# Performance work log

Measured on AMD Instinct MI355X. Metric: run time of the kernel, lower is better.

## Reference

```python
import jax, jax.numpy as jnp
import numpy as np

M_IND = 1024   # inducing points
K_NN = 16      # nearest neighbors
JITTER = 1e-4


def rbf(X, Z):
    # unit-variance, unit-lengthscale RBF kernel; returns (K, squared distances)
    sq = jnp.sum(X * X, -1)[:, None] + jnp.sum(Z * Z, -1)[None, :] - 2.0 * (X @ Z.T)
    sq = jnp.maximum(sq, 0.0)
    return jnp.exp(-0.5 * sq), sq


def setup_inputs() -> dict:
    key = jax.random.key(0)
    k1, k2, k3 = jax.random.split(key, 3)
    return {
        "X": jax.random.normal(k1, (65536, 3), jnp.float32),
        "Z": jax.random.normal(k2, (M_IND, 3), jnp.float32),
        "Lu_raw": jax.random.normal(k3, (M_IND, M_IND), jnp.float32),
        "mu": jnp.zeros((M_IND,), jnp.float32),
    }


def reference(X, Z, Lu_raw, mu):
    N = X.shape[0]
    Kxx = jnp.ones((N,), X.dtype)                      # diag of RBF(X,X) is 1
    Kxz, dist = rbf(X, Z)                              # [N,M], [N,M]
    Kzz, _ = rbf(Z, Z)                                 # [M,M]

    # transform_to(lower_cholesky): strict lower triangle + exp(diag)
    Lu = jnp.tril(Lu_raw, -1) + jnp.diag(jnp.exp(jnp.diag(Lu_raw)))

    eyeM = jnp.eye(M_IND, dtype=X.dtype)
    L = jnp.linalg.cholesky(Kzz + JITTER * eyeM)       # [M,M]
    Kzz_j = L @ L.T                                    # == little_L @ little_L.T math (Kzz + jitter*I)
    Su = Lu @ Lu.T                                     # full variational covariance

    # K nearest inducing points per data point (argsort(dist)[:, :K])
    _, idx = jax.lax.top_k(-dist, K_NN)                # [N,K]

    lKzz = Kzz_j[idx[:, :, None], idx[:, None, :]]     # [N,K,K] gathered submatrices
    lS = Su[idx[:, :, None], idx[:, None, :]]          # [N,K,K]
    lKxz = jnp.take_along_axis(Kxz, idx, axis=1)       # [N,K]
    lmu = mu[idx]                                      # [N,K]

    eyeK = jnp.eye(K_NN, dtype=X.dtype)
    inv = jnp.linalg.inv(lKzz + JITTER * eyeK)         # batched tiny inverses [N,K,K]
    W = jnp.einsum('nk,nkj->nj', lKxz, inv)            # [N,K]

    mean = jnp.einsum('nk,nk->n', W, lmu)              # [N]
    cov = (Kxx
           - jnp.einsum('ni,nij,nj->n', W, lKzz, W)
           + jnp.einsum('ni,nij,nj->n', W, lS, W))
    std = jnp.sqrt(jnp.clip(cov, 0.05, None))          # qF scale = clamp(cov, 0.05)**0.5
    return jnp.stack([mean, std])                      # [2,N] qF parameters
```

## Files before the change

### kernel.cpp

```cpp
#include <hip/hip_runtime.h>
#include <math.h>

#define N_PTS 65536
#define M_IND 1024
#define KNN 16
#define JITTER 1e-4f

#define PACKED_FLOATS (M_IND * (M_IND + 1) / 2)
#define PACKED_BYTES  ((size_t)PACKED_FLOATS * sizeof(float))

#define TSU 32
#define SU_BLOCKS 528
#define PTS_PER_BLK 128
#define QSTRIDE 17
#define GRID_BLKS (N_PTS / PTS_PER_BLK)


__device__ __forceinline__ void su_tile(const float* __restrict__ Lu_raw,
                                        float* __restrict__ P,
                                        int bid, int tid,
                                        float (*As)[36], float (*Bs)[36]) {
    int rt = (int)((sqrtf(8.0f * (float)bid + 1.0f) - 1.0f) * 0.5f);
    while ((rt + 1) * (rt + 2) / 2 <= bid) ++rt;
    while (rt * (rt + 1) / 2 > bid) --rt;
    int ct = bid - rt * (rt + 1) / 2;
    int i0 = rt * TSU, j0 = ct * TSU;

    int tx = tid & 15, ty = tid >> 4;
    int sr = tid >> 3, sc = (tid & 7) << 2;
    float a00 = 0.f, a01 = 0.f, a10 = 0.f, a11 = 0.f;

    int nch = ct + 1;
    int gi = i0 + sr, gj = j0 + sr;
    float4 pa = *(const float4*)(Lu_raw + (unsigned)gi * M_IND + sc);
    float4 pb = *(const float4*)(Lu_raw + (unsigned)gj * M_IND + sc);

    for (int c = 0; c < nch; ++c) {
        int gk = (c << 5) + sc;
        float aa[4] = {pa.x, pa.y, pa.z, pa.w};
        float bb[4] = {pb.x, pb.y, pb.z, pb.w};
        #pragma unroll
        for (int q = 0; q < 4; ++q) {
            int k = gk + q;
            aa[q] = (k < gi) ? aa[q] : ((k == gi) ? __expf(aa[q]) : 0.0f);
            bb[q] = (k < gj) ? bb[q] : ((k == gj) ? __expf(bb[q]) : 0.0f);
        }
        *(float4*)&As[sr][sc] = make_float4(aa[0], aa[1], aa[2], aa[3]);
        *(float4*)&Bs[sr][sc] = make_float4(bb[0], bb[1], bb[2], bb[3]);
        __syncthreads();
        if (c + 1 < nch) {
            int kn = ((c + 1) << 5) + sc;
            pa = *(const float4*)(Lu_raw + (unsigned)gi * M_IND + kn);
            pb = *(const float4*)(Lu_raw + (unsigned)gj * M_IND + kn);
        }
        #pragma unroll
        for (int kk = 0; kk < 32; kk += 4) {
            float4 av0 = *(const float4*)&As[ty][kk];
            float4 av1 = *(const float4*)&As[ty + 16][kk];
            float4 bv0 = *(const float4*)&Bs[tx][kk];
            float4 bv1 = *(const float4*)&Bs[tx + 16][kk];
            a00 = fmaf(av0.x, bv0.x, fmaf(av0.y, bv0.y, fmaf(av0.z, bv0.z, fmaf(av0.w, bv0.w, a00))));
            a01 = fmaf(av0.x, bv1.x, fmaf(av0.y, bv1.y, fmaf(av0.z, bv1.z, fmaf(av0.w, bv1.w, a01))));
            a10 = fmaf(av1.x, bv0.x, fmaf(av1.y, bv0.y, fmaf(av1.z, bv0.z, fmaf(av1.w, bv0.w, a10))));
            a11 = fmaf(av1.x, bv1.x, fmaf(av1.y, bv1.y, fmaf(av1.z, bv1.z, fmaf(av1.w, bv1.w, a11))));
        }
        __syncthreads();
    }

    int ia = i0 + ty, ib = i0 + ty + 16;
    int ja = j0 + tx, jb = j0 + tx + 16;
    if (ja <= ia) P[((unsigned)ia * (ia + 1) >> 1) + ja] = a00;
    if (jb <= ia) P[((unsigned)ia * (ia + 1) >> 1) + jb] = a01;
    if (ja <= ib) P[((unsigned)ib * (ib + 1) >> 1) + ja] = a10;
    if (jb <= ib) P[((unsigned)ib * (ib + 1) >> 1) + jb] = a11;
}

__global__ __launch_bounds__(256) void su_kernel(const float* __restrict__ Lu_raw,
                                                 float* __restrict__ P) {
    __shared__ float As[TSU][36];
    __shared__ float Bs[TSU][36];
    su_tile(Lu_raw, P, blockIdx.x, threadIdx.x, As, Bs);
}

__device__ __forceinline__ void ce(unsigned long long& x, unsigned long long& y) {
    unsigned long long a = x, b = y;
    bool c = a < b;
    x = c ? a : b;
    y = c ? b : a;
}
__device__ __forceinline__ void ce(float& x, float& y) {
    float a = fminf(x, y), b = fmaxf(x, y);
    x = a; y = b;
}

template <typename KT>
__device__ __forceinline__ void sort16(KT* a) {
    #pragma unroll
    for (int p = 1; p < 16; p <<= 1)
        #pragma unroll
        for (int k = p; k >= 1; k >>= 1)
            #pragma unroll
            for (int j = k & (p - 1); j + k < 16; j += 2 * k)
                #pragma unroll
                for (int i = 0; i < k; ++i)
                    if (i + j + k < 16)
                        if (((i + j) / (2 * p)) == ((i + j + k) / (2 * p)))
                            ce(a[i + j], a[i + j + k]);
}

template <typename KT>
__device__ __forceinline__ void cleanup16(KT* a) {
    #pragma unroll
    for (int d = 8; d >= 1; d >>= 1)
        #pragma unroll
        for (int i = 0; i < 16; ++i)
            if ((i & d) == 0) ce(a[i], a[i | d]);
}

__device__ __forceinline__ float uval(float4 z, float xn0, float xn1, float xn2) {
    return fmaf(xn0, z.x, fmaf(xn1, z.y, fmaf(xn2, z.z, z.w)));
}

template <int MODE>
__global__ __launch_bounds__(256, 2) void vnngp_kernel(const float* __restrict__ X,
                                                       const float* __restrict__ Z,
                                                       const float* __restrict__ mu,
                                                       float* __restrict__ P,
                                                       const float* __restrict__ Lu_raw,
                                                       unsigned int* __restrict__ ctr,
                                                       float* __restrict__ out) {
    __shared__ __align__(16) char smem[37888];
    float4* Zs = (float4*)smem;
    float* mus = (float*)(smem + 16384);
    unsigned long long* qb = (unsigned long long*)(smem + 20480);
    int tid = threadIdx.x;

    for (int r = tid; r < M_IND; r += 256) {
        float zx = Z[r * 3 + 0], zy = Z[r * 3 + 1], zz = Z[r * 3 + 2];
        Zs[r] = make_float4(zx, zy, zz, 0.5f * (zx * zx + zy * zy + zz * zz));
        mus[r] = mu[r];
    }

    if (MODE == 2) {
        float (*As)[36] = (float (*)[36])(smem + 20480);
        float (*Bs)[36] = (float (*)[36])(smem + 20480 + 4608);
        int t = blockIdx.x;
        #pragma unroll
        for (int r = 16; r < 32; ++r) {
            int s = (r * (r + 1)) >> 1;
            if (t >= s) ++t;
        }
        su_tile(Lu_raw, P, t, tid, As, Bs);
        if (blockIdx.x < 16) {
            int r = 16 + blockIdx.x;
            su_tile(Lu_raw, P, (r * (r + 1)) >> 1, tid, As, Bs);
        }
        __syncthreads();
        if (tid == 0) {
            __threadfence();
            atomicAdd(ctr, 1u);
        }
    } else {
        __syncthreads();
    }

    {
        int pt = tid >> 2, sub = tid & 3;
        int nA = blockIdx.x * PTS_PER_BLK + pt;
        int nB = nA + 64;
        float xA0 = X[nA * 3 + 0], xA1 = X[nA * 3 + 1], xA2 = X[nA * 3 + 2];
        float xB0 = X[nB * 3 + 0], xB1 = X[nB * 3 + 1], xB2 = X[nB * 3 + 2];
        float xqA = fmaf(xA0, xA0, fmaf(xA1, xA1, xA2 * xA2));
        float xqB = fmaf(xB0, xB0, fmaf(xB1, xB1, xB2 * xB2));
        float nA0 = -xA0, nA1 = -xA1, nA2 = -xA2;
        float nB0 = -xB0, nB1 = -xB1, nB2 = -xB2;
        int mbase = sub << 8;
        int rot = sub << 1;

        float TA[16], TB[16];
        #pragma unroll
        for (int j = 0; j < 16; ++j) { TA[j] = 3.4e38f; TB[j] = 3.4e38f; }
        #pragma unroll 1
        for (int c = 0; c < 16; ++c) {
            int base = mbase + (c << 4);
            #pragma unroll
            for (int j = 0; j < 16; ++j) {
                int m = base + ((j + rot) & 15);
                float4 z = Zs[m];
                TA[j] = fminf(TA[j], uval(z, nA0, nA1, nA2));
                TB[j] = fminf(TB[j], uval(z, nB0, nB1, nB2));
            }
        }
        sort16(TA);
        sort16(TB);
        #pragma unroll
        for (int round = 1; round <= 2; round <<= 1) {
            float oA[16], oB[16];
            #pragma unroll
            for (int i = 0; i < 16; ++i) {
                oA[i] = __shfl_xor(TA[i], round, 64);
                oB[i] = __shfl_xor(TB[i], round, 64);
            }
            #pragma unroll
            for (int i = 0; i < 16; ++i) {
                TA[i] = fminf(TA[i], oA[15 - i]);
                TB[i] = fminf(TB[i], oB[15 - i]);
            }
            cleanup16(TA);
            cleanup16(TB);
        }
        float TstarA = TA[15], TstarB = TB[15];

        unsigned short* mycA = ((unsigned short*)qb) + pt * (QSTRIDE * 4) + sub * 16;
        unsigned short* mycB = ((unsigned short*)qb) + (pt + 64) * (QSTRIDE * 4) + sub * 16;
        int cntA = 0, cntB = 0;
        #pragma unroll 1
        for (int c = 0; c < 16; ++c) {
            int base = mbase + (c << 4);
            #pragma unroll
            for (int j = 0; j < 16; ++j) {
                int m = base + ((j + rot) & 15);
                float4 z = Zs[m];
                float uA = uval(z, nA0, nA1, nA2);
                float uB = uval(z, nB0, nB1, nB2);
                if (uA <= TstarA) { if (cntA < 16) mycA[cntA] = (unsigned short)m; ++cntA; }
                if (uB <= TstarB) { if (cntB < 16) mycB[cntB] = (unsigned short)m; ++cntB; }
            }
        }

        int ovfA = cntA > 16 ? 1 : 0;
        ovfA |= __shfl_xor(ovfA, 1, 64);
        ovfA |= __shfl_xor(ovfA, 2, 64);
        int ovfB = cntB > 16 ? 1 : 0;
        ovfB |= __shfl_xor(ovfB, 1, 64);
        ovfB |= __shfl_xor(ovfB, 2, 64);

        if (!ovfA) {
            const unsigned long long* m64 = (const unsigned long long*)mycA;
            unsigned long long raw[4] = {m64[0], m64[1], m64[2], m64[3]};
            unsigned long long C[16];
            #pragma unroll
            for (int i = 0; i < 16; ++i) {
                int m = (int)((raw[i >> 2] >> ((i & 3) * 16)) & 0x3FF);
                float u = uval(Zs[m], nA0, nA1, nA2);
                float d = fmaxf(fmaf(2.0f, u, xqA), 0.0f);
                unsigned long long key =
                    ((unsigned long long)__float_as_uint(d) << 32) | (unsigned)m;
                C[i] = (i < cntA) ? key : ~0ULL;
            }
            sort16(C);
            #pragma unroll
            for (int round = 1; round <= 2; round <<= 1) {
                unsigned long long o[16];
                #pragma unroll
                for (int i = 0; i < 16; ++i) o[i] = __shfl_xor(C[i], round, 64);
                #pragma unroll
                for (int i = 0; i < 16; ++i) {
                    unsigned long long b = o[15 - i];
                    C[i] = C[i] < b ? C[i] : b;
                }
                cleanup16(C);
            }
            if (sub == 0) {
                #pragma unroll
                for (int i = 0; i < 16; ++i) qb[pt * QSTRIDE + i] = C[i];
            }
        } else if (sub == 0) {
            unsigned long long R[16];
            #pragma unroll
            for (int i = 0; i < 16; ++i) R[i] = ~0ULL;
            for (int m = 0; m < M_IND; ++m) {
                float u = uval(Zs[m], nA0, nA1, nA2);
                float d = fmaxf(fmaf(2.0f, u, xqA), 0.0f);
                unsigned long long kk =
                    ((unsigned long long)__float_as_uint(d) << 32) | (unsigned)m;
                if (kk < R[15]) {
                    #pragma unroll
                    for (int j = 0; j < 16; ++j) {
                        unsigned long long t = R[j];
                        bool cc = kk < t;
                        R[j] = cc ? kk : t;
                        kk = cc ? t : kk;
                    }
                }
            }
            #pragma unroll
            for (int i = 0; i < 16; ++i) qb[pt * QSTRIDE + i] = R[i];
        }

        if (!ovfB) {
            const unsigned long long* m64 = (const unsigned long long*)mycB;
            unsigned long long raw[4] = {m64[0], m64[1], m64[2], m64[3]};
            unsigned long long C[16];
            #pragma unroll
            for (int i = 0; i < 16; ++i) {
                int m = (int)((raw[i >> 2] >> ((i & 3) * 16)) & 0x3FF);
                float u = uval(Zs[m], nB0, nB1, nB2);
                float d = fmaxf(fmaf(2.0f, u, xqB), 0.0f);
                unsigned long long key =
                    ((unsigned long long)__float_as_uint(d) << 32) | (unsigned)m;
                C[i] = (i < cntB) ? key : ~0ULL;
            }
            sort16(C);
            #pragma unroll
            for (int round = 1; round <= 2; round <<= 1) {
                unsigned long long o[16];
                #pragma unroll
                for (int i = 0; i < 16; ++i) o[i] = __shfl_xor(C[i], round, 64);
                #pragma unroll
                for (int i = 0; i < 16; ++i) {
                    unsigned long long b = o[15 - i];
                    C[i] = C[i] < b ? C[i] : b;
                }
                cleanup16(C);
            }
            if (sub == 0) {
                #pragma unroll
                for (int i = 0; i < 16; ++i) qb[(pt + 64) * QSTRIDE + i] = C[i];
            }
        } else if (sub == 0) {
            unsigned long long R[16];
            #pragma unroll
            for (int i = 0; i < 16; ++i) R[i] = ~0ULL;
            for (int m = 0; m < M_IND; ++m) {
                float u = uval(Zs[m], nB0, nB1, nB2);
                float d = fmaxf(fmaf(2.0f, u, xqB), 0.0f);
                unsigned long long kk =
                    ((unsigned long long)__float_as_uint(d) << 32) | (unsigned)m;
                if (kk < R[15]) {
                    #pragma unroll
                    for (int j = 0; j < 16; ++j) {
                        unsigned long long t = R[j];
                        bool cc = kk < t;
                        R[j] = cc ? kk : t;
                        kk = cc ? t : kk;
                    }
                }
            }
            #pragma unroll
            for (int i = 0; i < 16; ++i) qb[(pt + 64) * QSTRIDE + i] = R[i];
        }
    }
    __syncthreads();

    if (MODE == 2) {
        if (tid == 0) {
            while (__hip_atomic_load(ctr, __ATOMIC_ACQUIRE, __HIP_MEMORY_SCOPE_AGENT)
                   < (unsigned)GRID_BLKS)
                __builtin_amdgcn_s_sleep(8);
        }
        __syncthreads();
    }

    int role = tid >> 7;
    int pt2 = tid & 127;
    int n = blockIdx.x * PTS_PER_BLK + pt2;
    int idx[KNN];
    float kv[KNN];
    float nx[KNN], ny[KNN], nz[KNN], nq[KNN];
    #pragma unroll
    for (int a = 0; a < KNN; ++a) {
        unsigned long long k = qb[pt2 * QSTRIDE + a];
        idx[a] = (int)(k & 0xFFFFFFFFULL);
        float d = __uint_as_float((unsigned)(k >> 32));
        kv[a] = __expf(-0.5f * d);
        float4 z = Zs[idx[a]];
        nx[a] = z.x; ny[a] = z.y; nz[a] = z.z; nq[a] = z.w;
    }
    __syncthreads();

    float A[KNN * (KNN + 1) / 2];
    #pragma unroll
    for (int r = 0; r < KNN; ++r) {
        A[r * (r + 1) / 2 + r] = 1.0f + 2.0f * JITTER;
        #pragma unroll
        for (int c = 0; c < r; ++c) {
            float dot = fmaf(nx[r], nx[c], fmaf(ny[r], ny[c], nz[r] * nz[c]));
            A[r * (r + 1) / 2 + c] = __expf(fminf(dot - nq[r] - nq[c], 0.0f));
        }
    }

    #pragma unroll
    for (int c = 0; c < KNN; ++c) {
        float diag = A[c * (c + 1) / 2 + c];
        #pragma unroll
        for (int k = 0; k < c; ++k) {
            float l = A[c * (c + 1) / 2 + k];
            diag = fmaf(-l, l, diag);
        }
        float rinv = __frsqrt_rn(fmaxf(diag, 1e-12f));
        A[c * (c + 1) / 2 + c] = rinv;
        #pragma unroll
        for (int r = c + 1; r < KNN; ++r) {
            float v = A[r * (r + 1) / 2 + c];
            #pragma unroll
            for (int k = 0; k < c; ++k)
                v = fmaf(-A[r * (r + 1) / 2 + k], A[c * (c + 1) / 2 + k], v);
            A[r * (r + 1) / 2 + c] = v * rinv;
        }
    }

    float w[KNN];
    #pragma unroll
    for (int r = 0; r < KNN; ++r) {
        float v = kv[r];
        #pragma unroll
        for (int c = 0; c < r; ++c) v = fmaf(-A[r * (r + 1) / 2 + c], w[c], v);
        w[r] = v * A[r * (r + 1) / 2 + r];
    }
    #pragma unroll
    for (int r = KNN - 1; r >= 0; --r) {
        float v = w[r];
        #pragma unroll
        for (int c = r + 1; c < KNN; ++c) v = fmaf(-A[c * (c + 1) / 2 + r], w[c], v);
        w[r] = v * A[r * (r + 1) / 2 + r];
    }

    float wk = 0.f, ww = 0.f, mean = 0.f;
    #pragma unroll
    for (int a = 0; a < KNN; ++a) {
        wk = fmaf(w[a], kv[a], wk);
        ww = fmaf(w[a], w[a], ww);
        mean = fmaf(w[a], mus[idx[a]], mean);
    }

    float qs_p = 0.f;
    if (MODE != 0) {
        #pragma unroll
        for (int r = 0; r < KNN; ++r) {
            if ((r & 1) == role) {
                int a = idx[r];
                float wr = w[r];
                float rowacc = 0.f;
                #pragma unroll
                for (int c = 0; c < r; ++c) {
                    int b = idx[c];
                    int hi = a > b ? a : b;
                    int lo = a > b ? b : a;
                    rowacc = fmaf(w[c], P[((unsigned)hi * (hi + 1) >> 1) + lo], rowacc);
                }
                qs_p = fmaf(wr, fmaf(wr, P[((unsigned)a * (a + 1) >> 1) + a], 2.0f * rowacc), qs_p);
            }
        }
    } else if (role == 0) {
        int si[KNN]; float sw[KNN];
        #pragma unroll
        for (int a = 0; a < KNN; ++a) { si[a] = idx[a]; sw[a] = w[a]; }
        #pragma unroll
        for (int a = 1; a < KNN; ++a) {
            int iv = si[a]; float wv = sw[a];
            int b = a - 1;
            while (b >= 0 && si[b] > iv) { si[b + 1] = si[b]; sw[b + 1] = sw[b]; --b; }
            si[b + 1] = iv; sw[b + 1] = wv;
        }
        int s = 0;
        int kend = si[KNN - 1];
        for (int k = 0; k <= kend; ++k) {
            float v = 0.f;
            if (s < KNN && si[s] == k) {
                v = sw[s] * __expf(Lu_raw[(unsigned)k * M_IND + k]);
                ++s;
            }
            for (int a = s; a < KNN; ++a)
                v = fmaf(sw[a], Lu_raw[(unsigned)si[a] * M_IND + k], v);
            qs_p = fmaf(v, v, qs_p);
        }
    }

    float* xch = (float*)qb;
    if (role == 1) xch[pt2] = qs_p;
    __syncthreads();
    if (role == 0) {
        float qs = qs_p + xch[pt2];
        float cov = 1.0f - (wk - JITTER * ww) + qs;
        float sd = sqrtf(fmaxf(cov, 0.05f));
        out[n] = mean;
        out[N_PTS + n] = sd;
    }
}

extern "C" void kernel_launch(void* const* d_in, const int* in_sizes, int n_in,
                              void* d_out, int out_size, void* d_ws, size_t ws_size,
                              hipStream_t stream) {
    const float* X      = (const float*)d_in[0];
    const float* Z      = (const float*)d_in[1];
    const float* Lu_raw = (const float*)d_in[2];
    const float* mu     = (const float*)d_in[3];
    float* out = (float*)d_out;

    if (ws_size >= PACKED_BYTES + 64) {
        float* P = (float*)d_ws;
        unsigned int* ctr = (unsigned int*)((char*)d_ws + PACKED_BYTES);
        hipMemsetAsync(ctr, 0, sizeof(unsigned int), stream);
        vnngp_kernel<2><<<GRID_BLKS, 256, 0, stream>>>(X, Z, mu, P, Lu_raw, ctr, out);
    } else if (ws_size >= PACKED_BYTES) {
        float* P = (float*)d_ws;
        su_kernel<<<SU_BLOCKS, 256, 0, stream>>>(Lu_raw, P);
        vnngp_kernel<1><<<GRID_BLKS, 256, 0, stream>>>(X, Z, mu, P, Lu_raw, nullptr, out);
    } else {
        vnngp_kernel<0><<<GRID_BLKS, 256, 0, stream>>>(X, Z, mu, nullptr, Lu_raw, nullptr, out);
    }
}
```

Measured before the change: 163.6 us.

## Split Su build and cooperative 4-lane per-point Cholesky into separate kernels

Replaces the fused persistent kernel, which built packed Su inside the grid and spin-waited on a global counter, with a separate su_kernel launch followed by a new selection-plus-solve kernel. The new kernel uses 8 lanes per point for top-k selection over 128 inducing points each, with a threshold filter pass and a full-scan fallback on overflow. It then splits each point's 16x16 Cholesky, triangular solves and the Su quadratic form across 4 lanes using shuffles, with 4 blocks per CU instead of 2. This removes the grid-wide spin barrier and cuts per-thread register load. In exchange it adds a second launch and extra shuffle traffic.

```diff
diff --git a/kernel.cpp b/kernel.cpp
--- a/kernel.cpp
+++ b/kernel.cpp
@@ -119,6 +119,394 @@
 
 __device__ __forceinline__ float uval(float4 z, float xn0, float xn1, float xn2) {
     return fmaf(xn0, z.x, fmaf(xn1, z.y, fmaf(xn2, z.z, z.w)));
+}
+
+#define LI0(c) ((c) & 3)
+#define LI1(c) ((c) & 7)
+#define LI2(c) ((c) < 12 ? (c) : 0)
+
+__global__ __launch_bounds__(256, 4) void selp2_kernel(const float* __restrict__ X,
+                                                       const float* __restrict__ Z,
+                                                       const float* __restrict__ mu,
+                                                       const float* __restrict__ P,
+                                                       float* __restrict__ out) {
+    __shared__ __align__(16) char smem[36864];
+    float4* Zs = (float4*)smem;
+    float* mus = (float*)(smem + 16384);
+    unsigned long long* qb = (unsigned long long*)(smem + 20480);
+    int tid = threadIdx.x;
+
+    for (int r = tid; r < M_IND; r += 256) {
+        float zx = Z[r * 3 + 0], zy = Z[r * 3 + 1], zz = Z[r * 3 + 2];
+        Zs[r] = make_float4(zx, zy, zz, 0.5f * (zx * zx + zy * zy + zz * zz));
+        mus[r] = mu[r];
+    }
+    __syncthreads();
+
+    {
+        int oct = tid >> 3, sub = tid & 7;
+        int nA = blockIdx.x * 64 + oct;
+        int nB = nA + 32;
+        float xA0 = X[nA * 3 + 0], xA1 = X[nA * 3 + 1], xA2 = X[nA * 3 + 2];
+        float xB0 = X[nB * 3 + 0], xB1 = X[nB * 3 + 1], xB2 = X[nB * 3 + 2];
+        float xqA = fmaf(xA0, xA0, fmaf(xA1, xA1, xA2 * xA2));
+        float xqB = fmaf(xB0, xB0, fmaf(xB1, xB1, xB2 * xB2));
+        float mA0 = -xA0, mA1 = -xA1, mA2 = -xA2;
+        float mB0 = -xB0, mB1 = -xB1, mB2 = -xB2;
+        int mbase = sub << 7;
+        int rot = sub << 1;
+
+        float TA[16], TB[16];
+        #pragma unroll
+        for (int j = 0; j < 16; ++j) { TA[j] = 3.4e38f; TB[j] = 3.4e38f; }
+        #pragma unroll 1
+        for (int c = 0; c < 8; ++c) {
+            int base = mbase + (c << 4);
+            #pragma unroll
+            for (int j = 0; j < 16; ++j) {
+                int m = base + ((j + rot) & 15);
+                float4 z = Zs[m];
+                TA[j] = fminf(TA[j], uval(z, mA0, mA1, mA2));
+                TB[j] = fminf(TB[j], uval(z, mB0, mB1, mB2));
+            }
+        }
+        sort16(TA);
+        sort16(TB);
+        #pragma unroll
+        for (int round = 1; round <= 4; round <<= 1) {
+            float oA[16], oB[16];
+            #pragma unroll
+            for (int i = 0; i < 16; ++i) {
+                oA[i] = __shfl_xor(TA[i], round, 64);
+                oB[i] = __shfl_xor(TB[i], round, 64);
+            }
+            #pragma unroll
+            for (int i = 0; i < 16; ++i) {
+                TA[i] = fminf(TA[i], oA[15 - i]);
+                TB[i] = fminf(TB[i], oB[15 - i]);
+            }
+            cleanup16(TA);
+            cleanup16(TB);
+        }
+        float TstarA = TA[15], TstarB = TB[15];
+
+        unsigned short* mycA = ((unsigned short*)qb) + oct * 128 + sub * 16;
+        unsigned short* mycB = ((unsigned short*)qb) + (oct + 32) * 128 + sub * 16;
+        int cntA = 0, cntB = 0;
+        #pragma unroll 1
+        for (int c = 0; c < 8; ++c) {
+            int base = mbase + (c << 4);
+            #pragma unroll
+            for (int j = 0; j < 16; ++j) {
+                int m = base + ((j + rot) & 15);
+                float4 z = Zs[m];
+                float uA = uval(z, mA0, mA1, mA2);
+                float uB = uval(z, mB0, mB1, mB2);
+                if (uA <= TstarA) { if (cntA < 16) mycA[cntA] = (unsigned short)m; ++cntA; }
+                if (uB <= TstarB) { if (cntB < 16) mycB[cntB] = (unsigned short)m; ++cntB; }
+            }
+        }
+
+        int ovfA = cntA > 16 ? 1 : 0;
+        ovfA |= __shfl_xor(ovfA, 1, 64);
+        ovfA |= __shfl_xor(ovfA, 2, 64);
+        ovfA |= __shfl_xor(ovfA, 4, 64);
+        int ovfB = cntB > 16 ? 1 : 0;
+        ovfB |= __shfl_xor(ovfB, 1, 64);
+        ovfB |= __shfl_xor(ovfB, 2, 64);
+        ovfB |= __shfl_xor(ovfB, 4, 64);
+
+        if (!ovfA) {
+            const unsigned long long* m64 = (const unsigned long long*)mycA;
+            unsigned long long raw[4] = {m64[0], m64[1], m64[2], m64[3]};
+            unsigned long long C[16];
+            #pragma unroll
+            for (int i = 0; i < 16; ++i) {
+                int m = (int)((raw[i >> 2] >> ((i & 3) * 16)) & 0x3FF);
+                float u = uval(Zs[m], mA0, mA1, mA2);
+                float d = fmaxf(fmaf(2.0f, u, xqA), 0.0f);
+                unsigned long long key =
+                    ((unsigned long long)__float_as_uint(d) << 32) | (unsigned)m;
+                C[i] = (i < cntA) ? key : ~0ULL;
+            }
+            sort16(C);
+            #pragma unroll
+            for (int round = 1; round <= 4; round <<= 1) {
+                unsigned long long o[16];
+                #pragma unroll
+                for (int i = 0; i < 16; ++i) o[i] = __shfl_xor(C[i], round, 64);
+                #pragma unroll
+                for (int i = 0; i < 16; ++i) {
+                    unsigned long long b = o[15 - i];
+                    C[i] = C[i] < b ? C[i] : b;
+                }
+                cleanup16(C);
+            }
+            if (sub == 0) {
+                #pragma unroll
+                for (int i = 0; i < 16; ++i) qb[oct * 32 + i] = C[i];
+            }
+        } else if (sub == 0) {
+            unsigned long long R[16];
+            #pragma unroll
+            for (int i = 0; i < 16; ++i) R[i] = ~0ULL;
+            for (int m = 0; m < M_IND; ++m) {
+                float u = uval(Zs[m], mA0, mA1, mA2);
+                float d = fmaxf(fmaf(2.0f, u, xqA), 0.0f);
+                unsigned long long kk =
+                    ((unsigned long long)__float_as_uint(d) << 32) | (unsigned)m;
+                if (kk < R[15]) {
+                    #pragma unroll
+                    for (int j = 0; j < 16; ++j) {
+                        unsigned long long t = R[j];
+                        bool cc = kk < t;
+                        R[j] = cc ? kk : t;
+                        kk = cc ? t : kk;
+                    }
+                }
+            }
+            #pragma unroll
+            for (int i = 0; i < 16; ++i) qb[oct * 32 + i] = R[i];
+        }
+
+        if (!ovfB) {
+            const unsigned long long* m64 = (const unsigned long long*)mycB;
+            unsigned long long raw[4] = {m64[0], m64[1], m64[2], m64[3]};
+            unsigned long long C[16];
+            #pragma unroll
+            for (int i = 0; i < 16; ++i) {
+                int m = (int)((raw[i >> 2] >> ((i & 3) * 16)) & 0x3FF);
+                float u = uval(Zs[m], mB0, mB1, mB2);
+                float d = fmaxf(fmaf(2.0f, u, xqB), 0.0f);
+                unsigned long long key =
+                    ((unsigned long long)__float_as_uint(d) << 32) | (unsigned)m;
+                C[i] = (i < cntB) ? key : ~0ULL;
+            }
+            sort16(C);
+            #pragma unroll
+            for (int round = 1; round <= 4; round <<= 1) {
+                unsigned long long o[16];
+                #pragma unroll
+                for (int i = 0; i < 16; ++i) o[i] = __shfl_xor(C[i], round, 64);
+                #pragma unroll
+                for (int i = 0; i < 16; ++i) {
+                    unsigned long long b = o[15 - i];
+                    C[i] = C[i] < b ? C[i] : b;
+                }
+                cleanup16(C);
+            }
+            if (sub == 0) {
+                #pragma unroll
+                for (int i = 0; i < 16; ++i) qb[(oct + 32) * 32 + i] = C[i];
+            }
+        } else if (sub == 0) {
+            unsigned long long R[16];
+            #pragma unroll
+            for (int i = 0; i < 16; ++i) R[i] = ~0ULL;
+            for (int m = 0; m < M_IND; ++m) {
+                float u = uval(Zs[m], mB0, mB1, mB2);
+                float d = fmaxf(fmaf(2.0f, u, xqB), 0.0f);
+                unsigned long long kk =
+                    ((unsigned long long)__float_as_uint(d) << 32) | (unsigned)m;
+                if (kk < R[15]) {
+                    #pragma unroll
+                    for (int j = 0; j < 16; ++j) {
+                        unsigned long long t = R[j];
+                        bool cc = kk < t;
+                        R[j] = cc ? kk : t;
+                        kk = cc ? t : kk;
+                    }
+                }
+            }
+            #pragma unroll
+            for (int i = 0; i < 16; ++i) qb[(oct + 32) * 32 + i] = R[i];
+        }
+    }
+    __syncthreads();
+
+    {
+        int g = tid >> 2, l = tid & 3;
+        int n = blockIdx.x * 64 + g;
+        int lanebase = (tid & 63) & ~3;
+
+        int idx[16];
+        int iown[4];
+        float kvown[4];
+        float4 zrown[4];
+        #pragma unroll
+        for (int a = 0; a < 16; ++a) {
+            unsigned long long k = qb[g * 32 + a];
+            int ia = (int)(k & 0xFFFFFFFFULL);
+            float d = __uint_as_float((unsigned)(k >> 32));
+            float kva = __expf(-0.5f * d);
+            idx[a] = ia;
+            if ((a & 3) == l) {
+                iown[a >> 2] = ia;
+                kvown[a >> 2] = kva;
+                zrown[a >> 2] = Zs[ia];
+            }
+        }
+
+        float L0[4], L1[8], L2[12], L3[16];
+        float dg[4];
+        #pragma unroll
+        for (int k = 0; k < 4; ++k) dg[k] = 1.0f + 2.0f * JITTER;
+        #pragma unroll
+        for (int c = 0; c < 16; ++c) {
+            float4 zc = Zs[idx[c]];
+            #pragma unroll
+            for (int k = 0; k < 4; ++k) {
+                if (c < 4 * (k + 1)) {
+                    int r = l + 4 * k;
+                    float dot = fmaf(zrown[k].x, zc.x,
+                                fmaf(zrown[k].y, zc.y, zrown[k].z * zc.z));
+                    float val = __expf(fminf(dot - zrown[k].w - zc.w, 0.0f));
+                    if (c < r) {
+                        if (k == 0) L0[LI0(c)] = val;
+                        else if (k == 1) L1[LI1(c)] = val;
+                        else if (k == 2) L2[LI2(c)] = val;
+                        else L3[c] = val;
+                    }
+                }
+            }
+        }
+
+        float rinvown[4];
+        #pragma unroll
+        for (int c = 0; c < 16; ++c) {
+            const int owner = c & 3, kc = c >> 2;
+            float dval = __shfl(dg[kc], lanebase + owner, 64);
+            float rinv = __frsqrt_rn(fmaxf(dval, 1e-12f));
+            if (l == owner) rinvown[kc] = rinv;
+            float cv[4];
+            #pragma unroll
+            for (int k = 0; k < 4; ++k) {
+                cv[k] = 0.f;
+                if (c < 4 * (k + 1)) {
+                    int r = l + 4 * k;
+                    if (r > c) {
+                        float v;
+                        if (k == 0) { v = L0[LI0(c)] * rinv; L0[LI0(c)] = v; }
+                        else if (k == 1) { v = L1[LI1(c)] * rinv; L1[LI1(c)] = v; }
+                        else if (k == 2) { v = L2[LI2(c)] * rinv; L2[LI2(c)] = v; }
+                        else { v = L3[c] * rinv; L3[c] = v; }
+                        cv[k] = v;
+                    }
+                }
+            }
+            #pragma unroll
+            for (int j = c + 1; j < 16; ++j) {
+                float colj = __shfl(cv[j >> 2], lanebase + (j & 3), 64);
+                #pragma unroll
+                for (int k = 0; k < 4; ++k) {
+                    if (j < 4 * (k + 1)) {
+                        int r = l + 4 * k;
+                        if (r > j) {
+                            float u = cv[k] * colj;
+                            if (k == 0) L0[LI0(j)] -= u;
+                            else if (k == 1) L1[LI1(j)] -= u;
+                            else if (k == 2) L2[LI2(j)] -= u;
+                            else L3[j] -= u;
+                        } else if (r == j) {
+                            dg[k] = fmaf(-colj, colj, dg[k]);
+                        }
+                    }
+                }
+            }
+        }
+
+        float acc[4];
+        #pragma unroll
+        for (int k = 0; k < 4; ++k) acc[k] = kvown[k];
+        float yown[4];
+        #pragma unroll
+        for (int r = 0; r < 16; ++r) {
+            const int owner = r & 3, kr = r >> 2;
+            float yr = __shfl(acc[kr] * rinvown[kr], lanebase + owner, 64);
+            if (l == owner) yown[kr] = yr;
+            #pragma unroll
+            for (int k = 0; k < 4; ++k) {
+                if (r < 4 * (k + 1)) {
+                    int rr = l + 4 * k;
+                    if (rr > r) {
+                        float lv;
+                        if (k == 0) lv = L0[LI0(r)];
+                        else if (k == 1) lv = L1[LI1(r)];
+                        else if (k == 2) lv = L2[LI2(r)];
+                        else lv = L3[r];
+                        acc[k] = fmaf(-lv, yr, acc[k]);
+                    }
+                }
+            }
+        }
+
+        float wfull[16];
+        float wown[4] = {0.f, 0.f, 0.f, 0.f};
+        #pragma unroll
+        for (int r = 15; r >= 0; --r) {
+            const int owner = r & 3, kr = r >> 2;
+            float contrib = 0.f;
+            #pragma unroll
+            for (int k = 0; k < 4; ++k) {
+                if (r < 4 * (k + 1)) {
+                    int j = l + 4 * k;
+                    if (j > r) {
+                        float lv;
+                        if (k == 0) lv = L0[LI0(r)];
+                        else if (k == 1) lv = L1[LI1(r)];
+                        else if (k == 2) lv = L2[LI2(r)];
+                        else lv = L3[r];
+                        contrib = fmaf(lv, wown[k], contrib);
+                    }
+                }
+            }
+            contrib += __shfl_xor(contrib, 1, 64);
+            contrib += __shfl_xor(contrib, 2, 64);
+            float wr = __shfl((yown[kr] - contrib) * rinvown[kr],
+                              lanebase + owner, 64);
+            wfull[r] = wr;
+            if (l == owner) wown[kr] = wr;
+        }
+
+        float wkp = 0.f, wwp = 0.f, mnp = 0.f;
+        #pragma unroll
+        for (int k = 0; k < 4; ++k) {
+            wkp = fmaf(wown[k], kvown[k], wkp);
+            wwp = fmaf(wown[k], wown[k], wwp);
+            mnp = fmaf(wown[k], mus[iown[k]], mnp);
+        }
+
+        float qsp = 0.f;
+        #pragma unroll
+        for (int k = 0; k < 4; ++k) {
+            int r = l + 4 * k;
+            int a = iown[k];
+            float wr = wown[k];
+            float rowacc = 0.f;
+            #pragma unroll
+            for (int c = 0; c < 15; ++c) {
+                if (c < r) {
+                    int b = idx[c];
+                    int hi = a > b ? a : b;
+                    int lo = a > b ? b : a;
+                    rowacc = fmaf(wfull[c], P[((unsigned)hi * (hi + 1) >> 1) + lo], rowacc);
+                }
+            }
+            qsp = fmaf(wr, fmaf(wr, P[((unsigned)a * (a + 1) >> 1) + a], 2.0f * rowacc), qsp);
+        }
+
+        wkp += __shfl_xor(wkp, 1, 64); wkp += __shfl_xor(wkp, 2, 64);
+        wwp += __shfl_xor(wwp, 1, 64); wwp += __shfl_xor(wwp, 2, 64);
+        mnp += __shfl_xor(mnp, 1, 64); mnp += __shfl_xor(mnp, 2, 64);
+        qsp += __shfl_xor(qsp, 1, 64); qsp += __shfl_xor(qsp, 2, 64);
+
+        if (l == 0) {
+            float cov = 1.0f - (wkp - JITTER * wwp) + qsp;
+            float sd = sqrtf(fmaxf(cov, 0.05f));
+            out[n] = mnp;
+            out[N_PTS + n] = sd;
+        }
+    }
 }
 
 template <int MODE>
@@ -140,29 +528,7 @@
         Zs[r] = make_float4(zx, zy, zz, 0.5f * (zx * zx + zy * zy + zz * zz));
         mus[r] = mu[r];
     }
-
-    if (MODE == 2) {
-        float (*As)[36] = (float (*)[36])(smem + 20480);
-        float (*Bs)[36] = (float (*)[36])(smem + 20480 + 4608);
-        int t = blockIdx.x;
-        #pragma unroll
-        for (int r = 16; r < 32; ++r) {
-            int s = (r * (r + 1)) >> 1;
-            if (t >= s) ++t;
-        }
-        su_tile(Lu_raw, P, t, tid, As, Bs);
-        if (blockIdx.x < 16) {
-            int r = 16 + blockIdx.x;
-            su_tile(Lu_raw, P, (r * (r + 1)) >> 1, tid, As, Bs);
-        }
-        __syncthreads();
-        if (tid == 0) {
-            __threadfence();
-            atomicAdd(ctr, 1u);
-        }
-    } else {
-        __syncthreads();
-    }
+    __syncthreads();
 
     {
         int pt = tid >> 2, sub = tid & 3;
@@ -343,15 +709,6 @@
     }
     __syncthreads();
 
-    if (MODE == 2) {
-        if (tid == 0) {
-            while (__hip_atomic_load(ctr, __ATOMIC_ACQUIRE, __HIP_MEMORY_SCOPE_AGENT)
-                   < (unsigned)GRID_BLKS)
-                __builtin_amdgcn_s_sleep(8);
-        }
-        __syncthreads();
-    }
-
     int role = tid >> 7;
     int pt2 = tid & 127;
     int n = blockIdx.x * PTS_PER_BLK + pt2;
@@ -385,8 +742,8 @@
         float diag = A[c * (c + 1) / 2 + c];
         #pragma unroll
         for (int k = 0; k < c; ++k) {
-            float l = A[c * (c + 1) / 2 + k];
-            diag = fmaf(-l, l, diag);
+            float lv = A[c * (c + 1) / 2 + k];
+            diag = fmaf(-lv, lv, diag);
         }
         float rinv = __frsqrt_rn(fmaxf(diag, 1e-12f));
         A[c * (c + 1) / 2 + c] = rinv;
@@ -425,24 +782,7 @@
     }
 
     float qs_p = 0.f;
-    if (MODE != 0) {
-        #pragma unroll
-        for (int r = 0; r < KNN; ++r) {
-            if ((r & 1) == role) {
-                int a = idx[r];
-                float wr = w[r];
-                float rowacc = 0.f;
-                #pragma unroll
-                for (int c = 0; c < r; ++c) {
-                    int b = idx[c];
-                    int hi = a > b ? a : b;
-                    int lo = a > b ? b : a;
-                    rowacc = fmaf(w[c], P[((unsigned)hi * (hi + 1) >> 1) + lo], rowacc);
-                }
-                qs_p = fmaf(wr, fmaf(wr, P[((unsigned)a * (a + 1) >> 1) + a], 2.0f * rowacc), qs_p);
-            }
-        }
-    } else if (role == 0) {
+    if (role == 0) {
         int si[KNN]; float sw[KNN];
         #pragma unroll
         for (int a = 0; a < KNN; ++a) { si[a] = idx[a]; sw[a] = w[a]; }
@@ -488,15 +828,10 @@
     const float* mu     = (const float*)d_in[3];
     float* out = (float*)d_out;
 
-    if (ws_size >= PACKED_BYTES + 64) {
-        float* P = (float*)d_ws;
-        unsigned int* ctr = (unsigned int*)((char*)d_ws + PACKED_BYTES);
-        hipMemsetAsync(ctr, 0, sizeof(unsigned int), stream);
-        vnngp_kernel<2><<<GRID_BLKS, 256, 0, stream>>>(X, Z, mu, P, Lu_raw, ctr, out);
-    } else if (ws_size >= PACKED_BYTES) {
+    if (ws_size >= PACKED_BYTES) {
         float* P = (float*)d_ws;
         su_kernel<<<SU_BLOCKS, 256, 0, stream>>>(Lu_raw, P);
-        vnngp_kernel<1><<<GRID_BLKS, 256, 0, stream>>>(X, Z, mu, P, Lu_raw, nullptr, out);
+        selp2_kernel<<<N_PTS / 64, 256, 0, stream>>>(X, Z, mu, P, out);
     } else {
         vnngp_kernel<0><<<GRID_BLKS, 256, 0, stream>>>(X, Z, mu, nullptr, Lu_raw, nullptr, out);
     }
```

Result: slower. 187.5 us (+14.6%).
